# Kernel tuning notes

Measured on AMD Instinct MI355X. Metric: run time of the kernel, lower is better.

The kernel has to match this reference:

```python
import jax, jax.numpy as jnp
import numpy as np

N_NODES = 50000
N_EDGES = 800000
X_DIM = 64
STATE_DIM = 64
IN_DIM = X_DIM + STATE_DIM
OUT_DIM = 64
N_HEADS = 4
HEAD_DIM = OUT_DIM // N_HEADS
NEG_SLOPE = 0.2


def setup_inputs() -> dict:
    key = jax.random.key(0)
    ks = jax.random.split(key, 7)
    x = jax.random.normal(ks[0], (N_NODES, X_DIM), dtype=jnp.float32)
    state = jax.random.normal(ks[1], (N_NODES, STATE_DIM), dtype=jnp.float32)
    edge_index = jax.random.randint(ks[2], (2, N_EDGES), 0, N_NODES, dtype=jnp.int64)
    edge_weight = jax.random.uniform(ks[3], (N_EDGES,), dtype=jnp.float32)
    # xavier-uniform-like scales
    w_scale = float(np.sqrt(2.0 / (IN_DIM + OUT_DIM)))
    a_scale = float(np.sqrt(2.0 / (N_HEADS + HEAD_DIM)))
    W = jax.random.normal(ks[4], (OUT_DIM, IN_DIM), dtype=jnp.float32) * w_scale
    attn_src = jax.random.normal(ks[5], (N_HEADS, HEAD_DIM), dtype=jnp.float32) * a_scale
    attn_dst = jax.random.normal(ks[6], (N_HEADS, HEAD_DIM), dtype=jnp.float32) * a_scale
    return {"x": x, "state": state, "edge_index": edge_index, "edge_weight": edge_weight,
            "W": W, "attn_src": attn_src, "attn_dst": attn_dst}


def reference(x, state, edge_index, edge_weight, W, attn_src, attn_dst):
    # edge_weight is ignored by design (pure attention behavior)
    del edge_weight
    N = x.shape[0]
    H, D = attn_src.shape
    # linear_in (no bias): [N, IN_DIM] @ [IN_DIM, OUT_DIM]
    h_flat = jnp.concatenate([x, state], axis=-1) @ W.T          # [N, OUT_DIM]
    h = h_flat.reshape(N, H, D)                                   # [N, H, D]
    src = edge_index[0]
    dst = edge_index[1]
    # per-node attention scores, then gather per-edge (same math as gathering h first)
    s_src = jnp.einsum('nhd,hd->nh', h, attn_src)                 # [N, H]
    s_dst = jnp.einsum('nhd,hd->nh', h, attn_dst)                 # [N, H]
    logits = s_src[src] + s_dst[dst]                              # [E, H]
    logits = jnp.where(logits >= 0, logits, NEG_SLOPE * logits)   # leaky_relu
    # segment softmax over incoming edges of each dst node (stable, two-pass)
    max_by_dst = jax.ops.segment_max(logits, dst, num_segments=N) # [N, H]
    exp_shifted = jnp.exp(logits - max_by_dst[dst])               # [E, H]
    denom = jax.ops.segment_sum(exp_shifted, dst, num_segments=N) # [N, H]
    alpha = exp_shifted / (denom[dst] + 1e-12)                    # [E, H]
    # weighted message aggregation
    msg = h[src] * alpha[:, :, None]                              # [E, H, D]
    out_flat = jax.ops.segment_sum(msg.reshape(msg.shape[0], H * D), dst, num_segments=N)
    out_flat = out_flat + h_flat                                  # residual (shapes always match)
    out_flat = jax.nn.elu(out_flat)                               # activation
    return out_flat
```

## Files before the change

### kernel.cpp

```cpp
#include <hip/hip_runtime.h>
#include <hip/hip_bf16.h>

#define N_NODES 50000
#define N_EDGES 800000
#define NBK 196
#define BCAP 40
#define CAP  4864

typedef __attribute__((ext_vector_type(8))) short bf16x8;
typedef __attribute__((ext_vector_type(4))) float f32x4;

__device__ __forceinline__ unsigned short f2bu(float f) {
    __hip_bfloat16 hb = __float2bfloat16(f);
    return *(unsigned short*)&hb;
}
__device__ __forceinline__ unsigned pk2(float a, float b) {
    return (unsigned)f2bu(a) | ((unsigned)f2bu(b) << 16);
}

__global__ void __launch_bounds__(256, 4)
k1_mfma(const float* __restrict__ x, const float* __restrict__ state,
        const float* __restrict__ W, const float* __restrict__ a_src,
        const float* __restrict__ a_dst,
        float* __restrict__ hf32, float* __restrict__ s_src4,
        float* __restrict__ s_dst4, int* __restrict__ gcur) {
    __shared__ unsigned short alds[64 * 136];
    __shared__ unsigned short wlds[64 * 136];
    int tid = threadIdx.x;
    int nb = blockIdx.x * 64;

    if (blockIdx.x == 0 && tid < NBK) gcur[tid] = 0;

    const float4* x4  = (const float4*)x;
    const float4* st4 = (const float4*)state;
    const float4* W4  = (const float4*)W;
    for (int idx = tid; idx < 2048; idx += 256) {
        int row = idx >> 5, qc = idx & 31;
        int n = nb + row;
        float4 v = make_float4(0.f, 0.f, 0.f, 0.f);
        if (n < N_NODES)
            v = (qc < 16) ? x4[(long)n * 16 + qc] : st4[(long)n * 16 + (qc - 16)];
        unsigned* ap = (unsigned*)&alds[row * 136 + qc * 4];
        ap[0] = pk2(v.x, v.y);
        ap[1] = pk2(v.z, v.w);
        float4 wv = W4[idx];
        unsigned* wp = (unsigned*)&wlds[row * 136 + qc * 4];
        wp[0] = pk2(wv.x, wv.y);
        wp[1] = pk2(wv.z, wv.w);
    }
    __syncthreads();

    int lane = tid & 63;
    int w = tid >> 6;
    int lrow = lane & 15, lq = lane >> 4;

    f32x4 acc[4];
#pragma unroll
    for (int c = 0; c < 4; ++c) acc[c] = (f32x4){0.f, 0.f, 0.f, 0.f};

#pragma unroll
    for (int kc = 0; kc < 4; ++kc) {
        bf16x8 af = *(const bf16x8*)&alds[(w * 16 + lrow) * 136 + kc * 32 + lq * 8];
#pragma unroll
        for (int c = 0; c < 4; ++c) {
            bf16x8 bf = *(const bf16x8*)&wlds[(c * 16 + lrow) * 136 + kc * 32 + lq * 8];
            acc[c] = __builtin_amdgcn_mfma_f32_16x16x32_bf16(af, bf, acc[c], 0, 0, 0);
        }
    }
    __syncthreads();

    float* hst = (float*)alds;
#pragma unroll
    for (int r = 0; r < 4; ++r) {
        int nl = w * 16 + lq * 4 + r;
#pragma unroll
        for (int c = 0; c < 4; ++c)
            hst[nl * 68 + c * 16 + lrow] = acc[c][r];
    }
    __syncthreads();

    int node = tid >> 2, chunk = tid & 3;
    int n = nb + node;
    if (n < N_NODES) {
        const float* hp = &hst[node * 68 + chunk * 16];
        float hv[16];
        float vs = 0.f, vd = 0.f;
#pragma unroll
        for (int i = 0; i < 16; ++i) {
            hv[i] = hp[i];
            vs = fmaf(hv[i], a_src[chunk * 16 + i], vs);
            vd = fmaf(hv[i], a_dst[chunk * 16 + i], vd);
        }
        float* dst = hf32 + (long)n * 64 + chunk * 16;
        *(float4*)(dst + 0)  = make_float4(hv[0],  hv[1],  hv[2],  hv[3]);
        *(float4*)(dst + 4)  = make_float4(hv[4],  hv[5],  hv[6],  hv[7]);
        *(float4*)(dst + 8)  = make_float4(hv[8],  hv[9],  hv[10], hv[11]);
        *(float4*)(dst + 12) = make_float4(hv[12], hv[13], hv[14], hv[15]);
        s_src4[(long)nb * 4 + tid] = vs;
        s_dst4[(long)nb * 4 + tid] = vd;
    }
}

__global__ void __launch_bounds__(256)
k_bin(const int* __restrict__ ei, int* __restrict__ gcur, int* __restrict__ recs) {
    __shared__ int cnt[NBK];
    __shared__ int stage[NBK][BCAP];
    int tid = threadIdx.x;
    for (int i = tid; i < NBK; i += 256) cnt[i] = 0;
    __syncthreads();
    int e0 = blockIdx.x * 4096;
#pragma unroll
    for (int k = 0; k < 4; ++k) {
        int e = e0 + k * 1024 + tid * 4;
        if (e < N_EDGES) {
            int4 sv = *(const int4*)(ei + e);
            int4 dv = *(const int4*)(ei + N_EDGES + e);
            int ss[4] = {sv.x, sv.y, sv.z, sv.w};
            int dd[4] = {dv.x, dv.y, dv.z, dv.w};
#pragma unroll
            for (int j = 0; j < 4; ++j) {
                int b = dd[j] >> 8;
                int rec = ss[j] | ((dd[j] & 255) << 16);
                int p = atomicAdd(&cnt[b], 1);
                if (p < BCAP) stage[b][p] = rec;
                else {
                    int g = atomicAdd(&gcur[b], 1);
                    recs[b * CAP + g] = rec;
                }
            }
        }
    }
    __syncthreads();
    for (int b = tid; b < NBK; b += 256) {
        int nb = min(cnt[b], BCAP);
        if (nb > 0) {
            int g = atomicAdd(&gcur[b], nb);
            int d0 = b * CAP + g;
            for (int i = 0; i < nb; ++i) recs[d0 + i] = stage[b][i];
        }
    }
}

__global__ void __launch_bounds__(256)
k_sort(const int* __restrict__ recs, const int* __restrict__ gcur,
       int* __restrict__ recs2, int* __restrict__ off, int* __restrict__ deg) {
    __shared__ int cnt[256];
    __shared__ int pos[256];
    __shared__ int wsum[4];
    int tid = threadIdx.x, b = blockIdx.x;
    cnt[tid] = 0;
    __syncthreads();
    int base = b * CAP, cntb = gcur[b];
    for (int i = tid; i < cntb; i += 256)
        atomicAdd(&cnt[(recs[base + i] >> 16) & 255], 1);
    __syncthreads();
    int lane = tid & 63, wid = tid >> 6;
    int v = cnt[tid], inc = v;
#pragma unroll
    for (int s = 1; s < 64; s <<= 1) {
        int t = __shfl_up(inc, s);
        if (lane >= s) inc += t;
    }
    if (lane == 63) wsum[wid] = inc;
    __syncthreads();
    if (tid == 0) {
        int s = 0;
#pragma unroll
        for (int w = 0; w < 4; ++w) { int t = wsum[w]; wsum[w] = s; s += t; }
    }
    __syncthreads();
    int excl = wsum[wid] + inc - v;
    pos[tid] = excl;
    int n = b * 256 + tid;
    if (n < N_NODES) { off[n] = base + excl; deg[n] = v; }
    __syncthreads();
    for (int i = tid; i < cntb; i += 256) {
        int r = recs[base + i];
        int p = atomicAdd(&pos[(r >> 16) & 255], 1);
        recs2[base + p] = r & 0xFFFF;
    }
}

__global__ void k_agg(const int* __restrict__ off, const int* __restrict__ deg,
                      const int* __restrict__ csr, const float* __restrict__ s_src4,
                      const float* __restrict__ s_dst4,
                      const float* __restrict__ hf32, float* __restrict__ out) {
    int wave = threadIdx.x >> 6, lane = threadIdx.x & 63;
    int n = blockIdx.x * 4 + wave;
    if (n >= N_NODES) return;
    int q = lane >> 3, d = lane & 7, hh = d >> 1;
    int b = off[n], nE = deg[n];
    float sdh = s_dst4[(long)n * 4 + hh];

    float den = 0.f;
    float a0 = 0, a1 = 0, a2 = 0, a3 = 0, a4 = 0, a5 = 0, a6 = 0, a7 = 0;
    for (int c = 0; c < nE; c += 64) {
        int jn = min(64, nE - c);
        int svl = (lane < jn) ? csr[b + c + lane] : 0;
        for (int j = 0; j < jn; j += 8) {
            int myj = j + q;
            int s = __shfl(svl, myj);
            if (myj < jn) {
                float l = s_src4[s * 4 + hh] + sdh;
                float ex = __expf(fmaxf(l, 0.2f * l));
                den += ex;
                const float4* hp = (const float4*)(hf32 + (long)s * 64 + 8 * d);
                float4 h0 = hp[0], h1 = hp[1];
                a0 = fmaf(ex, h0.x, a0); a1 = fmaf(ex, h0.y, a1);
                a2 = fmaf(ex, h0.z, a2); a3 = fmaf(ex, h0.w, a3);
                a4 = fmaf(ex, h1.x, a4); a5 = fmaf(ex, h1.y, a5);
                a6 = fmaf(ex, h1.z, a6); a7 = fmaf(ex, h1.w, a7);
            }
        }
    }
#pragma unroll
    for (int o2 = 8; o2 < 64; o2 <<= 1) {
        den += __shfl_xor(den, o2);
        a0 += __shfl_xor(a0, o2);
        a1 += __shfl_xor(a1, o2);
        a2 += __shfl_xor(a2, o2);
        a3 += __shfl_xor(a3, o2);
        a4 += __shfl_xor(a4, o2);
        a5 += __shfl_xor(a5, o2);
        a6 += __shfl_xor(a6, o2);
        a7 += __shfl_xor(a7, o2);
    }

    if (q == 0) {
        const float4* hrp = (const float4*)(hf32 + (long)n * 64 + 8 * d);
        float4 r0 = hrp[0], r1 = hrp[1];
        float inv = 1.0f / (den + 1e-12f);
        float o0 = a0 * inv + r0.x, o1 = a1 * inv + r0.y;
        float o2 = a2 * inv + r0.z, o3 = a3 * inv + r0.w;
        float o4 = a4 * inv + r1.x, o5 = a5 * inv + r1.y;
        float o6 = a6 * inv + r1.z, o7 = a7 * inv + r1.w;
        o0 = (o0 > 0.f) ? o0 : __expf(o0) - 1.f;
        o1 = (o1 > 0.f) ? o1 : __expf(o1) - 1.f;
        o2 = (o2 > 0.f) ? o2 : __expf(o2) - 1.f;
        o3 = (o3 > 0.f) ? o3 : __expf(o3) - 1.f;
        o4 = (o4 > 0.f) ? o4 : __expf(o4) - 1.f;
        o5 = (o5 > 0.f) ? o5 : __expf(o5) - 1.f;
        o6 = (o6 > 0.f) ? o6 : __expf(o6) - 1.f;
        o7 = (o7 > 0.f) ? o7 : __expf(o7) - 1.f;
        float* op = &out[(long)n * 64 + 8 * d];
        *(float4*)(op + 0) = make_float4(o0, o1, o2, o3);
        *(float4*)(op + 4) = make_float4(o4, o5, o6, o7);
    }
}

extern "C" void kernel_launch(void* const* d_in, const int* in_sizes, int n_in,
                              void* d_out, int out_size, void* d_ws, size_t ws_size,
                              hipStream_t stream) {
    const float* x      = (const float*)d_in[0];
    const float* state  = (const float*)d_in[1];
    const int*   ei     = (const int*)d_in[2];
    const float* W      = (const float*)d_in[4];
    const float* a_src  = (const float*)d_in[5];
    const float* a_dst  = (const float*)d_in[6];

    float* out = (float*)d_out;

    float* hf32   = (float*)d_ws;
    float* s_src4 = hf32 + (long)N_NODES * 64;
    float* s_dst4 = s_src4 + (long)N_NODES * 4;
    int*   gcur   = (int*)(s_dst4 + (long)N_NODES * 4);
    int*   off    = gcur + 256;
    int*   deg    = off + N_NODES;
    int*   recs   = deg + N_NODES;
    int*   recs2  = recs + (long)NBK * CAP;

    k1_mfma<<<782, 256, 0, stream>>>(x, state, W, a_src, a_dst,
                                     hf32, s_src4, s_dst4, gcur);
    k_bin<<<196, 256, 0, stream>>>(ei, gcur, recs);
    k_sort<<<NBK, 256, 0, stream>>>(recs, gcur, recs2, off, deg);
    k_agg<<<(N_NODES + 3) / 4, 256, 0, stream>>>(off, deg, recs2, s_src4, s_dst4, hf32, out);
}
```

Measured before the change: 73.69 us.

## Precompute per-edge attention exponentials in a separate kernel before aggregation

Adds a k_alpha kernel that computes the leaky-relu exponentials for all four heads of each sorted edge and writes them to a per-edge alpha buffer. k_sort now keeps the destination bits in each record so that kernel can recover the destination. The aggregation kernel then reads alpha contiguously instead of gathering s_src per edge and recomputing exp, and it drops the divergent branch. The cost is an extra launch and roughly 12.8MB of alpha write and read traffic, plus a small extra workspace region.

```diff
diff --git a/kernel.cpp b/kernel.cpp
--- a/kernel.cpp
+++ b/kernel.cpp
@@ -177,40 +177,60 @@
     for (int i = tid; i < cntb; i += 256) {
         int r = recs[base + i];
         int p = atomicAdd(&pos[(r >> 16) & 255], 1);
-        recs2[base + p] = r & 0xFFFF;
-    }
+        recs2[base + p] = r;
+    }
+}
+
+__global__ void __launch_bounds__(256)
+k_alpha(const int* __restrict__ recs2, const int* __restrict__ gcur,
+        const float* __restrict__ s_src4, const float* __restrict__ s_dst4,
+        float* __restrict__ alpha) {
+    int i = blockIdx.x * 256 + threadIdx.x;
+    int b = i / CAP;
+    int local = i - b * CAP;
+    if (local >= gcur[b]) return;
+    int r = recs2[i];
+    int src = r & 0xFFFF;
+    int dst = b * 256 + ((r >> 16) & 255);
+    float4 ss = *(const float4*)&s_src4[(long)src * 4];
+    float4 sd = *(const float4*)&s_dst4[(long)dst * 4];
+    float l0 = ss.x + sd.x, l1 = ss.y + sd.y;
+    float l2 = ss.z + sd.z, l3 = ss.w + sd.w;
+    float4 a;
+    a.x = __expf(fmaxf(l0, 0.2f * l0));
+    a.y = __expf(fmaxf(l1, 0.2f * l1));
+    a.z = __expf(fmaxf(l2, 0.2f * l2));
+    a.w = __expf(fmaxf(l3, 0.2f * l3));
+    *(float4*)&alpha[(long)i * 4] = a;
 }
 
 __global__ void k_agg(const int* __restrict__ off, const int* __restrict__ deg,
-                      const int* __restrict__ csr, const float* __restrict__ s_src4,
-                      const float* __restrict__ s_dst4,
+                      const int* __restrict__ csr, const float* __restrict__ alpha,
                       const float* __restrict__ hf32, float* __restrict__ out) {
     int wave = threadIdx.x >> 6, lane = threadIdx.x & 63;
     int n = blockIdx.x * 4 + wave;
     if (n >= N_NODES) return;
-    int q = lane >> 3, d = lane & 7, hh = d >> 1;
+    int q = lane >> 3, d = lane & 7;
+    int alane = q * 4 + ((d >> 1));
     int b = off[n], nE = deg[n];
-    float sdh = s_dst4[(long)n * 4 + hh];
 
     float den = 0.f;
     float a0 = 0, a1 = 0, a2 = 0, a3 = 0, a4 = 0, a5 = 0, a6 = 0, a7 = 0;
     for (int c = 0; c < nE; c += 64) {
         int jn = min(64, nE - c);
-        int svl = (lane < jn) ? csr[b + c + lane] : 0;
+        int svl = (lane < jn) ? (csr[b + c + lane] & 0xFFFF) : 0;
         for (int j = 0; j < jn; j += 8) {
             int myj = j + q;
             int s = __shfl(svl, myj);
-            if (myj < jn) {
-                float l = s_src4[s * 4 + hh] + sdh;
-                float ex = __expf(fmaxf(l, 0.2f * l));
-                den += ex;
-                const float4* hp = (const float4*)(hf32 + (long)s * 64 + 8 * d);
-                float4 h0 = hp[0], h1 = hp[1];
-                a0 = fmaf(ex, h0.x, a0); a1 = fmaf(ex, h0.y, a1);
-                a2 = fmaf(ex, h0.z, a2); a3 = fmaf(ex, h0.w, a3);
-                a4 = fmaf(ex, h1.x, a4); a5 = fmaf(ex, h1.y, a5);
-                a6 = fmaf(ex, h1.z, a6); a7 = fmaf(ex, h1.w, a7);
-            }
+            float av = alpha[(long)(b + c + j) * 4 + alane];
+            float ex = (myj < jn) ? av : 0.f;
+            den += ex;
+            const float4* hp = (const float4*)(hf32 + (long)s * 64 + 8 * d);
+            float4 h0 = hp[0], h1 = hp[1];
+            a0 = fmaf(ex, h0.x, a0); a1 = fmaf(ex, h0.y, a1);
+            a2 = fmaf(ex, h0.z, a2); a3 = fmaf(ex, h0.w, a3);
+            a4 = fmaf(ex, h1.x, a4); a5 = fmaf(ex, h1.y, a5);
+            a6 = fmaf(ex, h1.z, a6); a7 = fmaf(ex, h1.w, a7);
         }
     }
 #pragma unroll
@@ -268,10 +288,12 @@
     int*   deg    = off + N_NODES;
     int*   recs   = deg + N_NODES;
     int*   recs2  = recs + (long)NBK * CAP;
+    float* alpha  = (float*)(recs2 + (long)NBK * CAP);
 
     k1_mfma<<<782, 256, 0, stream>>>(x, state, W, a_src, a_dst,
                                      hf32, s_src4, s_dst4, gcur);
     k_bin<<<196, 256, 0, stream>>>(ei, gcur, recs);
     k_sort<<<NBK, 256, 0, stream>>>(recs, gcur, recs2, off, deg);
-    k_agg<<<(N_NODES + 3) / 4, 256, 0, stream>>>(off, deg, recs2, s_src4, s_dst4, hf32, out);
-}
+    k_alpha<<<(NBK * CAP) / 256, 256, 0, stream>>>(recs2, gcur, s_src4, s_dst4, alpha);
+    k_agg<<<(N_NODES + 3) / 4, 256, 0, stream>>>(off, deg, recs2, alpha, hf32, out);
+}
```

Measured after the change: 80.65 us. 1.09x slower.
